# Performance work log

Hardware: AMD Instinct MI355X
Metric: run time of the kernel (lower is better)

## Reference

```python
import jax, jax.numpy as jnp
import numpy as np

BN_EPS = 1e-6
SOFTMAX_EPS = 1e-8
D = 64      # fingerprint_dim
BD = 12     # bond_dim
N_ATOM = 10000
N_EDGE = 40000


def _bn(x, gamma, beta, mean, var):
    # BatchNorm1d in inference mode (running stats)
    return (x - mean) / jnp.sqrt(var + BN_EPS) * gamma + beta


def setup_inputs() -> dict:
    key = jax.random.key(0)
    ks = jax.random.split(key, 16)
    inp = {
        "atom": jax.random.normal(ks[0], (N_ATOM, D), dtype=jnp.float32),
        "bond_index": jax.random.randint(ks[1], (N_EDGE, 2), 0, N_ATOM, dtype=jnp.int64),
        "bond": jax.random.normal(ks[2], (N_EDGE, BD), dtype=jnp.float32),
        # encoder: Linear(bond_dim, D*D) + BatchNorm1d(D*D)
        "enc_W": jax.random.normal(ks[3], (D * D, BD), dtype=jnp.float32) * (1.0 / np.sqrt(BD)),
        "enc_b": jnp.zeros((D * D,), dtype=jnp.float32),
        "enc_gamma": jnp.ones((D * D,), dtype=jnp.float32),
        "enc_beta": jnp.zeros((D * D,), dtype=jnp.float32),
        "enc_mean": jnp.zeros((D * D,), dtype=jnp.float32),
        "enc_var": jnp.ones((D * D,), dtype=jnp.float32),
        # align: Linear(2*D, 1)
        "align_W": jax.random.normal(ks[4], (1, 2 * D), dtype=jnp.float32) * (1.0 / np.sqrt(2 * D)),
        "align_b": jnp.zeros((1,), dtype=jnp.float32),
        # attend: Linear(D, D) + BatchNorm1d(D), no activation
        "att_W": jax.random.normal(ks[5], (D, D), dtype=jnp.float32) * (1.0 / np.sqrt(D)),
        "att_b": jnp.zeros((D,), dtype=jnp.float32),
        "att_gamma": jnp.ones((D,), dtype=jnp.float32),
        "att_beta": jnp.zeros((D,), dtype=jnp.float32),
        "att_mean": jnp.zeros((D,), dtype=jnp.float32),
        "att_var": jnp.ones((D,), dtype=jnp.float32),
        # GRUCell(D, D)
        "gru_W_ih": jax.random.normal(ks[6], (3 * D, D), dtype=jnp.float32) * (1.0 / np.sqrt(D)),
        "gru_W_hh": jax.random.normal(ks[7], (3 * D, D), dtype=jnp.float32) * (1.0 / np.sqrt(D)),
        "gru_b_ih": jnp.zeros((3 * D,), dtype=jnp.float32),
        "gru_b_hh": jnp.zeros((3 * D,), dtype=jnp.float32),
    }
    return inp


def reference(atom, bond_index, bond,
              enc_W, enc_b, enc_gamma, enc_beta, enc_mean, enc_var,
              align_W, align_b,
              att_W, att_b, att_gamma, att_beta, att_mean, att_var,
              gru_W_ih, gru_W_hh, gru_b_ih, gru_b_hh):
    num_atom, d = atom.shape
    tgt = bond_index[:, 0]  # target atom of each edge
    nbr = bond_index[:, 1]  # neighbor atom of each edge

    # encoder: relu(BN(linear(bond))) -> per-edge [d, d] bond matrix
    enc = jax.nn.relu(_bn(bond @ enc_W.T + enc_b, enc_gamma, enc_beta, enc_mean, enc_var))
    enc = enc.reshape(-1, d, d)  # [E, d, d]

    # gather neighbor atoms, per-edge matvec through bond matrix
    neighbor = jnp.einsum('ed,edf->ef', atom[nbr], enc)  # [E, d]

    # attention logits (dropout is identity in eval)
    feat = jnp.concatenate([atom[tgt], neighbor], axis=-1)  # [E, 2d]
    score = jax.nn.leaky_relu(feat @ align_W.T + align_b, negative_slope=0.01)  # [E, 1]

    # segment softmax over target atoms
    mx = jax.ops.segment_max(score, tgt, num_segments=num_atom)  # [N, 1]
    ex = jnp.exp(score - mx[tgt])
    denom = jax.ops.segment_sum(ex, tgt, num_segments=num_atom)[tgt] + SOFTMAX_EPS
    attn = ex / denom  # [E, 1]

    # attend: BN(linear(neighbor)) (no activation), weighted scatter-add
    attd = _bn(neighbor @ att_W.T + att_b, att_gamma, att_beta, att_mean, att_var)
    context = jax.ops.segment_sum(attn * attd, tgt, num_segments=num_atom)  # [N, d]
    context = jax.nn.elu(context)

    # GRUCell(context, atom)
    gi = context @ gru_W_ih.T + gru_b_ih  # [N, 3d]
    gh = atom @ gru_W_hh.T + gru_b_hh     # [N, 3d]
    i_r, i_z, i_n = jnp.split(gi, 3, axis=-1)
    h_r, h_z, h_n = jnp.split(gh, 3, axis=-1)
    r = jax.nn.sigmoid(i_r + h_r)
    z = jax.nn.sigmoid(i_z + h_z)
    n = jnp.tanh(i_n + r * h_n)
    return (1.0 - z) * n + z * atom
```

## Files before the change

kernel.cpp:

```cpp
#include <hip/hip_runtime.h>
#include <math.h>

#define NA 10000
#define NE 40000

typedef float f2 __attribute__((ext_vector_type(2)));
typedef float f4 __attribute__((ext_vector_type(4)));
typedef float f16v __attribute__((ext_vector_type(16)));
typedef int   i4 __attribute__((ext_vector_type(4)));
typedef __bf16 bf16x8 __attribute__((ext_vector_type(8)));

union U8 { unsigned short us[8]; bf16x8 v; };
union UF4 { f4 v; f2 h[2]; };
union UC16 { f16v v; f2 h[8]; };

static __device__ __forceinline__ unsigned short bf_rne(float x){
  unsigned u = __float_as_uint(x);
  unsigned r = (u + 0x7fffu + ((u>>16)&1u)) >> 16;
  return (unsigned short)r;
}
static __device__ __forceinline__ float bf_to_f(unsigned short h){
  return __uint_as_float(((unsigned)h)<<16);
}
static __device__ __forceinline__ float rcpf(float x){
  float r; asm("v_rcp_f32 %0, %1" : "=v"(r) : "v"(x)); return r;
}
static __device__ __forceinline__ float fsig(float x){
  return rcpf(1.f + __expf(-x));
}
static __device__ __forceinline__ float ftanh(float x){
  float ax = fabsf(x);
  float e = __expf(ax + ax);
  float t = 1.f - 2.f*rcpf(e + 1.f);
  return copysignf(t, x);
}

__global__ __launch_bounds__(256) void k_pre(
  const float* __restrict__ encW, const float* __restrict__ encB,
  const float* __restrict__ eg, const float* __restrict__ ebt,
  const float* __restrict__ e_mn, const float* __restrict__ e_vr,
  const float* __restrict__ attW, const float* __restrict__ attB,
  const float* __restrict__ agm, const float* __restrict__ abt,
  const float* __restrict__ amn, const float* __restrict__ avr,
  const float* __restrict__ wih, const float* __restrict__ whh,
  const int* __restrict__ bidx, const float* __restrict__ atom,
  const float* __restrict__ alW,
  unsigned short* __restrict__ Bh, unsigned short* __restrict__ Bl,
  unsigned short* __restrict__ aBh, unsigned short* __restrict__ aBl,
  float* __restrict__ attBf, float* __restrict__ wT,
  float* __restrict__ p, int* __restrict__ cnt)
{
  int tid = threadIdx.x;
  int gid = blockIdx.x*256 + tid;
  int gstride = gridDim.x*256;
  for (int i=gid; i<65536; i+=gstride){
    int j = i&7, ll = (i>>3)&63, t = i>>9;
    int d = t>>1, ft = t&1;
    int k = ((ll>>5)<<3)+j;
    int n = d*64 + ft*32 + (ll&31);
    float s = eg[n]*rsqrtf(e_vr[n]+1e-6f);
    unsigned short vh=0, vl=0;
    if (k<12){
      float wv = encW[n*12+k]*s;
      unsigned short hi = bf_rne(wv);
      vh = hi; vl = bf_rne(wv - bf_to_f(hi));
    } else if (k==12){
      float b = (encB[n]-e_mn[n])*s + ebt[n];
      unsigned short hi = bf_rne(b);
      vh = hi; vl = bf_rne(b - bf_to_f(hi));
    }
    Bh[i] = vh; Bl[i] = vl;
  }
  for (int i=gid; i<4096; i+=gstride){
    int j=i&7, l=(i>>3)&63, t=i>>9;
    int kk=t>>1, nt=t&1;
    int k = kk*16 + ((l>>5)<<3) + j;
    int n = nt*32 + (l&31);
    float s = agm[n]*rsqrtf(avr[n]+1e-6f);
    float wv = attW[n*64+k]*s;
    unsigned short hi = bf_rne(wv);
    aBh[i]=hi; aBl[i]=bf_rne(wv - bf_to_f(hi));
  }
  for (int f=gid; f<64; f+=gstride){
    float s = agm[f]*rsqrtf(avr[f]+1e-6f);
    attBf[f] = (attB[f]-amn[f])*s + abt[f];
  }
  for (int i=gid; i<24576; i+=gstride){
    int j=i&3, f=(i>>2)&63, idx2=i>>8;
    int g=idx2>>4, kg=idx2&15, k=kg*4+j;
    wT[i] = (g<3)? wih[(g*64+f)*64+k] : whh[((g-3)*64+f)*64+k];
  }
  {
    int wid = gid>>6;
    int l = tid&63;
    float wl = alW[l];
    for (int a=wid; a<NA; a+=(gstride>>6)){
      float v = wl*atom[(size_t)a*64+l];
      v += __shfl_xor(v,1);  v += __shfl_xor(v,2);
      v += __shfl_xor(v,4);  v += __shfl_xor(v,8);
      v += __shfl_xor(v,16); v += __shfl_xor(v,32);
      if (l==0) p[a]=v;
    }
  }
  for (int e=gid; e<NE; e+=gstride) atomicAdd(&cnt[bidx[e*2]],1);
}

__global__ __launch_bounds__(256) void k_scan(const int* __restrict__ cnt,
                                              int* __restrict__ rowstart,
                                              int* __restrict__ wofs)
{
  __shared__ int sPart[256];
  int t = threadIdx.x;
  int base = t*40;
  i4 buf[10];
  int sum = 0;
  if (base < NA){
    const i4* cp = (const i4*)(cnt + base);
    #pragma unroll
    for (int i=0;i<10;i++) buf[i] = cp[i];
    #pragma unroll
    for (int i=0;i<10;i++) sum += buf[i].x+buf[i].y+buf[i].z+buf[i].w;
  }
  sPart[t]=sum;
  __syncthreads();
  for (int off=1; off<256; off<<=1){
    int v = (t>=off)? sPart[t-off] : 0;
    __syncthreads();
    sPart[t]+=v;
    __syncthreads();
  }
  int run = sPart[t]-sum;
  if (base < NA){
    #pragma unroll
    for (int i=0;i<10;i++){
      i4 b=buf[i], o;
      o.x=run; run+=b.x; o.y=run; run+=b.y;
      o.z=run; run+=b.z; o.w=run; run+=b.w;
      ((i4*)(rowstart+base))[i]=o;
      ((i4*)(wofs+base))[i]=o;
    }
  }
  if (t==0) rowstart[NA]=NE;
}

__global__ __launch_bounds__(256) void k_scatter(const int* __restrict__ bidx,
                                                 int* __restrict__ wofs,
                                                 int* __restrict__ elist)
{
  int e = blockIdx.x*256 + threadIdx.x;
  if (e < NE){
    int tg = bidx[e*2];
    int pos = atomicAdd(&wofs[tg],1);
    elist[pos]=e;
  }
}

__global__ __launch_bounds__(256) void k_edge(
  const float* __restrict__ atom, const int* __restrict__ bidx, const float* __restrict__ bond,
  const unsigned short* __restrict__ Bh, const unsigned short* __restrict__ Bl,
  const unsigned short* __restrict__ aBh, const unsigned short* __restrict__ aBl,
  const float* __restrict__ alW,
  const int* __restrict__ elist, float* __restrict__ zC, float* __restrict__ qv)
{
  __shared__ float sA[4352];
  __shared__ float sP[8192];
  __shared__ int   sEl[64];
  __shared__ int   sNbr[64];

  int tid = threadIdx.x;
  int l = tid & 63;
  int w = tid >> 6;
  int g = l >> 5;
  int em = l & 31;
  int E0 = blockIdx.x * 64;

  if (tid < 64){
    int e = elist[E0+tid];
    sEl[tid] = e;
    sNbr[tid] = bidx[e*2+1];
  }
  __syncthreads();
  for (int i=tid; i<4096; i+=256){
    int le=i>>6, d=i&63;
    sA[d*68+le] = atom[(size_t)sNbr[le]*64 + d];
  }

  U8 A1[2], A2[2];
  #pragma unroll
  for (int t=0;t<2;t++){
    const f4* bp = (const f4*)(bond + (size_t)sEl[t*32+em]*12);
    f4 b0=bp[0], b1v=bp[1], b2v=bp[2];
    float bv[12] = {b0.x,b0.y,b0.z,b0.w,b1v.x,b1v.y,b1v.z,b1v.w,b2v.x,b2v.y,b2v.z,b2v.w};
    unsigned short hi[12], lo2[12];
    #pragma unroll
    for (int j=0;j<12;j++){ hi[j]=bf_rne(bv[j]); lo2[j]=bf_rne(bv[j]-bf_to_f(hi[j])); }
    #pragma unroll
    for (int j=0;j<8;j++){
      int k = g*8+j;
      A1[t].us[j] = (k<12)? hi[k] : (k==12? (unsigned short)0x3F80 : (unsigned short)0);
      A2[t].us[j] = (k<12)? lo2[k] : (unsigned short)0;
    }
  }
  __syncthreads();

  int ft = w & 1;
  int dbase = (w >> 1) * 32;

  f2 nacc[2][8];
  #pragma unroll
  for (int t=0;t<2;t++)
    #pragma unroll
    for (int i=0;i<8;i++) nacc[t][i] = (f2){0.f,0.f};
  f16v cz;
  #pragma unroll
  for (int r=0;r<16;r++) cz[r] = 0.f;

  const bf16x8* pH = (const bf16x8*)Bh + ((size_t)(dbase*2+ft)*64 + l);
  const bf16x8* pL = (const bf16x8*)Bl + ((size_t)(dbase*2+ft)*64 + l);
  U8 b0h, b0l, b1h, b1l;
  b0h.v = pH[0];   b0l.v = pL[0];
  b1h.v = pH[128]; b1l.v = pL[128];

  #pragma unroll 4
  for (int dd=0; dd<32; dd++){
    int d = dbase + dd;
    U8 b2h, b2l;
    b2h.v = pH[(dd+2)*128];
    b2l.v = pL[(dd+2)*128];

    UF4 ldA[2][4];
    #pragma unroll
    for (int t=0;t<2;t++)
      #pragma unroll
      for (int q=0;q<4;q++) ldA[t][q].v = *(const f4*)&sA[d*68 + t*32 + 8*q + 4*g];

    #pragma unroll
    for (int t=0;t<2;t++){
      UC16 c;
      c.v = __builtin_amdgcn_mfma_f32_32x32x16_bf16(A1[t].v, b0h.v, cz, 0,0,0);
      c.v = __builtin_amdgcn_mfma_f32_32x32x16_bf16(A2[t].v, b0h.v, c.v, 0,0,0);
      c.v = __builtin_amdgcn_mfma_f32_32x32x16_bf16(A1[t].v, b0l.v, c.v, 0,0,0);
      #pragma unroll
      for (int i=0;i<8;i++){
        f2 ev;
        ev[0] = fmaxf(c.h[i][0], 0.f);
        ev[1] = fmaxf(c.h[i][1], 0.f);
        asm("v_pk_fma_f32 %0, %1, %2, %0"
            : "+v"(nacc[t][i])
            : "v"(ldA[t][i>>1].h[i&1]), "v"(ev));
      }
    }
    b0h = b1h; b0l = b1l; b1h = b2h; b1l = b2l;
  }

  __syncthreads();
  {
    int dh = w >> 1;
    #pragma unroll
    for (int t=0;t<2;t++)
      #pragma unroll
      for (int r=0;r<16;r++)
        sP[(((dh*2+ft)*2+t)*16 + r)*64 + l] = nacc[t][r>>1][r&1];
  }
  __syncthreads();
  {
    int ftw = w&1, tw = w>>1;
    #pragma unroll
    for (int r=0;r<16;r++){
      float v = sP[(((0*2+ftw)*2+tw)*16 + r)*64 + l]
              + sP[(((1*2+ftw)*2+tw)*16 + r)*64 + l];
      int m = tw*32 + (r&3) + ((r>>2)<<3) + (g<<2);
      sA[m*68 + (ftw<<5) + em] = v;
    }
  }
  __syncthreads();

  {
    f16v c, c2;
    #pragma unroll
    for (int r=0;r<16;r++){ c[r] = 0.f; c2[r] = 0.f; }
    int mt2 = w>>1, nt = w&1;
    #pragma unroll
    for (int kk=0; kk<4; kk++){
      const float* src = &sA[(mt2*32+em)*68 + kk*16 + g*8];
      f4 x0 = *(const f4*)src;
      f4 x1 = *(const f4*)(src+4);
      U8 Ah, Al;
      #pragma unroll
      for (int j=0;j<4;j++){
        unsigned short h0 = bf_rne(x0[j]);
        Ah.us[j] = h0; Al.us[j] = bf_rne(x0[j]-bf_to_f(h0));
        unsigned short h1 = bf_rne(x1[j]);
        Ah.us[4+j] = h1; Al.us[4+j] = bf_rne(x1[j]-bf_to_f(h1));
      }
      U8 bh, bl;
      bh.v = *(const bf16x8*)(aBh + ((size_t)((kk*2+nt)*64 + l))*8);
      bl.v = *(const bf16x8*)(aBl + ((size_t)((kk*2+nt)*64 + l))*8);
      c = __builtin_amdgcn_mfma_f32_32x32x16_bf16(Ah.v, bh.v, c, 0,0,0);
      c = __builtin_amdgcn_mfma_f32_32x32x16_bf16(Al.v, bh.v, c, 0,0,0);
      c = __builtin_amdgcn_mfma_f32_32x32x16_bf16(Ah.v, bl.v, c, 0,0,0);
      if (nt){
        U8 qbh, qbl;
        #pragma unroll
        for (int j=0;j<8;j++){
          float v = alW[64 + kk*16 + (g<<3) + j];
          unsigned short hq = bf_rne(v);
          qbh.us[j] = (em==0)? hq : (unsigned short)0;
          qbl.us[j] = (em==0)? bf_rne(v - bf_to_f(hq)) : (unsigned short)0;
        }
        c2 = __builtin_amdgcn_mfma_f32_32x32x16_bf16(Ah.v, qbh.v, c2, 0,0,0);
        c2 = __builtin_amdgcn_mfma_f32_32x32x16_bf16(Al.v, qbh.v, c2, 0,0,0);
        c2 = __builtin_amdgcn_mfma_f32_32x32x16_bf16(Ah.v, qbl.v, c2, 0,0,0);
      }
    }
    #pragma unroll
    for (int r=0;r<16;r++){
      int row = (r&3) + ((r>>2)<<3) + ((l>>5)<<2);
      zC[(size_t)(E0 + mt2*32 + row)*64 + nt*32 + (l&31)] = c[r];
    }
    if (nt && em==0){
      #pragma unroll
      for (int r=0;r<16;r++){
        int row = (r&3) + ((r>>2)<<3) + (g<<2);
        qv[E0 + mt2*32 + row] = c2[r];
      }
    }
  }
}

__global__ __launch_bounds__(256, 4) void k_gru(
  const float* __restrict__ atom, const float* __restrict__ zC,
  const int* __restrict__ rowstart, const float* __restrict__ p,
  const float* __restrict__ qv, const float* __restrict__ alB,
  const float* __restrict__ attBf, const float* __restrict__ wT,
  const float* __restrict__ bih, const float* __restrict__ bhh,
  float* __restrict__ out)
{
  __shared__ float sc[4][4][64];
  __shared__ float shh[4][4][64];
  __shared__ float swT[6144];
  int tid = threadIdx.x;
  int l = tid & 63;
  int w = tid >> 6;
  int base = blockIdx.x*16 + w*4;
  float bias = attBf[l];
  float ab = alB[0];

  #pragma unroll
  for (int aa=0; aa<4; aa++){
    int a = base + aa;
    float hf = atom[(size_t)a*64 + l];
    float cf = 0.f;
    int d0 = rowstart[a];
    int deg = rowstart[a+1] - d0;
    if (deg > 0){
      float pa = p[a] + ab;
      float mx = -3e38f, dn = 0.f, y = 0.f;
      for (int i=0;i<deg;i++){
        float s = pa + qv[d0+i];
        s = (s>0.f)? s : 0.01f*s;
        float zc = zC[(size_t)(d0+i)*64 + l];
        if (s > mx){
          float al = __expf(mx - s);
          dn *= al; y *= al; mx = s;
        }
        float ex = __expf(s - mx);
        dn += ex;
        y = fmaf(ex, zc, y);
      }
      cf = (y + dn*bias)*rcpf(dn + 1e-8f);
      cf = (cf>0.f)? cf : expm1f(cf);
    }
    sc[w][aa][l] = cf; shh[w][aa][l] = hf;
  }

  float acc[6][4];
  #pragma unroll
  for (int gg=0;gg<6;gg++)
    #pragma unroll
    for (int aa=0;aa<4;aa++) acc[gg][aa]=0.f;

  for (int ch=0; ch<4; ch++){
    __syncthreads();
    #pragma unroll
    for (int ii=0; ii<6; ii++){
      int i = tid + ii*256;
      int f = i&63, q = i>>6; int gg = q>>2, kgc = q&3;
      ((f4*)swT)[i] = ((const f4*)wT)[(gg*16 + ch*4 + kgc)*64 + f];
    }
    __syncthreads();
    #pragma unroll
    for (int kgc=0; kgc<4; kgc++){
      int kg = ch*4 + kgc;
      f4 wv[6];
      #pragma unroll
      for (int gg=0;gg<6;gg++) wv[gg] = *(const f4*)&swT[((gg*4+kgc)*64 + l)*4];
      #pragma unroll
      for (int aa=0;aa<4;aa++){
        f4 cv = *(const f4*)&sc[w][aa][kg*4];
        f4 hv = *(const f4*)&shh[w][aa][kg*4];
        #pragma unroll
        for (int j=0;j<4;j++){
          acc[0][aa] = fmaf(cv[j], wv[0][j], acc[0][aa]);
          acc[1][aa] = fmaf(cv[j], wv[1][j], acc[1][aa]);
          acc[2][aa] = fmaf(cv[j], wv[2][j], acc[2][aa]);
          acc[3][aa] = fmaf(hv[j], wv[3][j], acc[3][aa]);
          acc[4][aa] = fmaf(hv[j], wv[4][j], acc[4][aa]);
          acc[5][aa] = fmaf(hv[j], wv[5][j], acc[5][aa]);
        }
      }
    }
  }

  float b0 = bih[l], b1 = bih[64+l], b2 = bih[128+l];
  float h0 = bhh[l], h1 = bhh[64+l], h2 = bhh[128+l];
  #pragma unroll
  for (int aa=0;aa<4;aa++){
    int a = base + aa;
    float hf = shh[w][aa][l];
    float r = fsig(acc[0][aa] + b0 + acc[3][aa] + h0);
    float z = fsig(acc[1][aa] + b1 + acc[4][aa] + h1);
    float n = ftanh(acc[2][aa] + b2 + r*(acc[5][aa] + h2));
    out[(size_t)a*64 + l] = (1.f - z)*n + z*hf;
  }
}

extern "C" void kernel_launch(void* const* d_in, const int* in_sizes, int n_in,
                              void* d_out, int out_size, void* d_ws, size_t ws_size,
                              hipStream_t stream) {
  const float* atom = (const float*)d_in[0];
  const int*   bidx = (const int*)  d_in[1];
  const float* bond = (const float*)d_in[2];
  const float* encW = (const float*)d_in[3];
  const float* encB = (const float*)d_in[4];
  const float* eg   = (const float*)d_in[5];
  const float* ebt  = (const float*)d_in[6];
  const float* e_mn = (const float*)d_in[7];
  const float* e_vr = (const float*)d_in[8];
  const float* alW  = (const float*)d_in[9];
  const float* alB  = (const float*)d_in[10];
  const float* atW  = (const float*)d_in[11];
  const float* atB  = (const float*)d_in[12];
  const float* agm  = (const float*)d_in[13];
  const float* abt  = (const float*)d_in[14];
  const float* amn  = (const float*)d_in[15];
  const float* avr  = (const float*)d_in[16];
  const float* wih  = (const float*)d_in[17];
  const float* whh  = (const float*)d_in[18];
  const float* bih  = (const float*)d_in[19];
  const float* bhh  = (const float*)d_in[20];

  float* ws = (float*)d_ws;
  unsigned short* Bh  = (unsigned short*)(ws + 0);
  unsigned short* Bl  = (unsigned short*)(ws + 32768);
  unsigned short* aBh = (unsigned short*)(ws + 65536);
  unsigned short* aBl = (unsigned short*)(ws + 67584);
  float* attBf   = ws + 69632;
  float* wT      = ws + 69696;
  float* p       = ws + 94272;
  int*   cnt     = (int*)(ws + 104288);
  int*   rowstart= (int*)(ws + 114304);
  int*   wofs    = (int*)(ws + 124320);
  int*   elist   = (int*)(ws + 134336);
  float* qv      = ws + 174336;
  float* zCb     = ws + 214336;
  float* outp    = (float*)d_out;

  hipMemsetAsync(cnt, 0, NA*sizeof(int), stream);
  k_pre<<<512, 256, 0, stream>>>(encW,encB,eg,ebt,e_mn,e_vr,
                                 atW,atB,agm,abt,amn,avr,
                                 wih,whh,bidx,atom,alW,
                                 Bh,Bl,aBh,aBl,attBf,wT,p,cnt);
  k_scan<<<1, 256, 0, stream>>>(cnt, rowstart, wofs);
  k_scatter<<<(NE+255)/256, 256, 0, stream>>>(bidx, wofs, elist);
  k_edge<<<625, 256, 0, stream>>>(atom, bidx, bond, Bh, Bl, aBh, aBl, alW,
                                  elist, zCb, qv);
  k_gru<<<625, 256, 0, stream>>>(atom, zCb, rowstart, p, qv, alB,
                                 attBf, wT, bih, bhh, outp);
}
```

Measured before the change: 180.8 us.

## Interleave hi/lo bf16 encoder weights and deepen edge-kernel prefetch pipeline

The hi and lo bf16 halves of the folded encoder weight are now stored interleaved in one buffer, so each lane fetches both halves with adjacent 16-byte loads. The register prefetch in k_edge grows from two to three stages using a rotating 4-slot array. The MFMA chain is wrapped in s_setprio to favour the matrix issue, and launch bounds request 3 blocks per CU. This targets latency on the weight stream in the edge kernel, at the cost of more registers per thread, which may clash with the occupancy hint. The rotating array indexed by dd&3 depends on full unrolling, or it may spill to scratch memory.

```diff
diff --git a/kernel.cpp b/kernel.cpp
--- a/kernel.cpp
+++ b/kernel.cpp
@@ -45,7 +45,7 @@
   const float* __restrict__ wih, const float* __restrict__ whh,
   const int* __restrict__ bidx, const float* __restrict__ atom,
   const float* __restrict__ alW,
-  unsigned short* __restrict__ Bh, unsigned short* __restrict__ Bl,
+  unsigned short* __restrict__ BI,
   unsigned short* __restrict__ aBh, unsigned short* __restrict__ aBl,
   float* __restrict__ attBf, float* __restrict__ wT,
   float* __restrict__ p, int* __restrict__ cnt)
@@ -53,23 +53,24 @@
   int tid = threadIdx.x;
   int gid = blockIdx.x*256 + tid;
   int gstride = gridDim.x*256;
-  for (int i=gid; i<65536; i+=gstride){
-    int j = i&7, ll = (i>>3)&63, t = i>>9;
+  for (int i=gid; i<131072; i+=gstride){
+    int j = i&15, ll = (i>>4)&63, t = i>>10;
     int d = t>>1, ft = t&1;
-    int k = ((ll>>5)<<3)+j;
+    int jj = j&7;
+    int k = ((ll>>5)<<3)+jj;
     int n = d*64 + ft*32 + (ll&31);
     float s = eg[n]*rsqrtf(e_vr[n]+1e-6f);
-    unsigned short vh=0, vl=0;
+    unsigned short outv = 0;
     if (k<12){
       float wv = encW[n*12+k]*s;
       unsigned short hi = bf_rne(wv);
-      vh = hi; vl = bf_rne(wv - bf_to_f(hi));
+      outv = (j<8)? hi : bf_rne(wv - bf_to_f(hi));
     } else if (k==12){
       float b = (encB[n]-e_mn[n])*s + ebt[n];
       unsigned short hi = bf_rne(b);
-      vh = hi; vl = bf_rne(b - bf_to_f(hi));
-    }
-    Bh[i] = vh; Bl[i] = vl;
+      outv = (j<8)? hi : bf_rne(b - bf_to_f(hi));
+    }
+    BI[i] = outv;
   }
   for (int i=gid; i<4096; i+=gstride){
     int j=i&7, l=(i>>3)&63, t=i>>9;
@@ -155,9 +156,9 @@
   }
 }
 
-__global__ __launch_bounds__(256) void k_edge(
+__global__ __launch_bounds__(256, 3) void k_edge(
   const float* __restrict__ atom, const int* __restrict__ bidx, const float* __restrict__ bond,
-  const unsigned short* __restrict__ Bh, const unsigned short* __restrict__ Bl,
+  const unsigned short* __restrict__ BI,
   const unsigned short* __restrict__ aBh, const unsigned short* __restrict__ aBl,
   const float* __restrict__ alW,
   const int* __restrict__ elist, float* __restrict__ zC, float* __restrict__ qv)
@@ -215,18 +216,17 @@
   #pragma unroll
   for (int r=0;r<16;r++) cz[r] = 0.f;
 
-  const bf16x8* pH = (const bf16x8*)Bh + ((size_t)(dbase*2+ft)*64 + l);
-  const bf16x8* pL = (const bf16x8*)Bl + ((size_t)(dbase*2+ft)*64 + l);
-  U8 b0h, b0l, b1h, b1l;
-  b0h.v = pH[0];   b0l.v = pL[0];
-  b1h.v = pH[128]; b1l.v = pL[128];
+  const bf16x8* pB = (const bf16x8*)BI + ((size_t)(dbase*2+ft)*64 + l)*2;
+  U8 rh[4], rl[4];
+  #pragma unroll
+  for (int s=0;s<3;s++){ rh[s].v = pB[s*256]; rl[s].v = pB[s*256+1]; }
 
   #pragma unroll 4
   for (int dd=0; dd<32; dd++){
     int d = dbase + dd;
-    U8 b2h, b2l;
-    b2h.v = pH[(dd+2)*128];
-    b2l.v = pL[(dd+2)*128];
+    int cs = dd&3, ns = (dd+3)&3;
+    rh[ns].v = pB[(size_t)(dd+3)*256];
+    rl[ns].v = pB[(size_t)(dd+3)*256 + 1];
 
     UF4 ldA[2][4];
     #pragma unroll
@@ -237,9 +237,11 @@
     #pragma unroll
     for (int t=0;t<2;t++){
       UC16 c;
-      c.v = __builtin_amdgcn_mfma_f32_32x32x16_bf16(A1[t].v, b0h.v, cz, 0,0,0);
-      c.v = __builtin_amdgcn_mfma_f32_32x32x16_bf16(A2[t].v, b0h.v, c.v, 0,0,0);
-      c.v = __builtin_amdgcn_mfma_f32_32x32x16_bf16(A1[t].v, b0l.v, c.v, 0,0,0);
+      __builtin_amdgcn_s_setprio(1);
+      c.v = __builtin_amdgcn_mfma_f32_32x32x16_bf16(A1[t].v, rh[cs].v, cz, 0,0,0);
+      c.v = __builtin_amdgcn_mfma_f32_32x32x16_bf16(A2[t].v, rh[cs].v, c.v, 0,0,0);
+      c.v = __builtin_amdgcn_mfma_f32_32x32x16_bf16(A1[t].v, rl[cs].v, c.v, 0,0,0);
+      __builtin_amdgcn_s_setprio(0);
       #pragma unroll
       for (int i=0;i<8;i++){
         f2 ev;
@@ -250,7 +252,6 @@
             : "v"(ldA[t][i>>1].h[i&1]), "v"(ev));
       }
     }
-    b0h = b1h; b0l = b1l; b1h = b2h; b1l = b2l;
   }
 
   __syncthreads();
@@ -451,8 +452,7 @@
   const float* bhh  = (const float*)d_in[20];
 
   float* ws = (float*)d_ws;
-  unsigned short* Bh  = (unsigned short*)(ws + 0);
-  unsigned short* Bl  = (unsigned short*)(ws + 32768);
+  unsigned short* BI  = (unsigned short*)(ws + 0);
   unsigned short* aBh = (unsigned short*)(ws + 65536);
   unsigned short* aBl = (unsigned short*)(ws + 67584);
   float* attBf   = ws + 69632;
@@ -470,10 +470,10 @@
   k_pre<<<512, 256, 0, stream>>>(encW,encB,eg,ebt,e_mn,e_vr,
                                  atW,atB,agm,abt,amn,avr,
                                  wih,whh,bidx,atom,alW,
-                                 Bh,Bl,aBh,aBl,attBf,wT,p,cnt);
+                                 BI,aBh,aBl,attBf,wT,p,cnt);
   k_scan<<<1, 256, 0, stream>>>(cnt, rowstart, wofs);
   k_scatter<<<(NE+255)/256, 256, 0, stream>>>(bidx, wofs, elist);
-  k_edge<<<625, 256, 0, stream>>>(atom, bidx, bond, Bh, Bl, aBh, aBl, alW,
+  k_edge<<<625, 256, 0, stream>>>(atom, bidx, bond, BI, aBh, aBl, alW,
                                   elist, zCb, qv);
   k_gru<<<625, 256, 0, stream>>>(atom, zCb, rowstart, p, qv, alB,
                                  attBf, wT, bih, bhh, outp);
```

Result: faster. 175.6 us (-2.9%).
